# Kernel optimization log

Hardware: AMD Instinct MI355X
Metric: run time of the kernel (lower is better)

The kernel has to match this reference:

```python
import jax, jax.numpy as jnp
import numpy as np

KERNEL_MUL = 2.0
KERNEL_NUM = 5
EPS = 1e-06


def setup_inputs() -> dict:
    key = jax.random.key(0)
    k1, k2 = jax.random.split(key)
    N, D = 4096, 256
    source = jax.random.normal(k1, (N, D), dtype=jnp.float32)
    target = jax.random.normal(k2, (N, D), dtype=jnp.float32)
    return {"source": source, "target": target}


def reference(source, target):
    n_src = source.shape[0]
    total = jnp.concatenate([source, target], axis=0)  # [2N, D]
    n = total.shape[0]
    # the broadcasted (total0 - total1)**2 sum, without the O(N^2*D) tensor).
    sq = jnp.sum(total * total, axis=1)  # [2N]
    L2 = sq[:, None] + sq[None, :] - 2.0 * (total @ total.T)  # [2N, 2N]
    # Bandwidth from detached distances (torch uses L2_distance.data).
    bandwidth = jax.lax.stop_gradient(jnp.sum(L2)) / (n * n - n)
    bandwidth = bandwidth / (KERNEL_MUL ** (KERNEL_NUM // 2))
    kernels = jnp.zeros_like(L2)
    for i in range(KERNEL_NUM):
        bw = bandwidth * (KERNEL_MUL ** i)
        kernels = kernels + jnp.exp(-L2 / (bw + EPS))
    XX = kernels[:n_src, :n_src]
    YY = kernels[n_src:, n_src:]
    XY = kernels[:n_src, n_src:]
    YX = kernels[n_src:, :n_src]
    return jnp.mean(XX + YY - XY - YX)
```

## Files before the change

kernel.cpp:

```cpp
#include <hip/hip_runtime.h>

#define N_TOT 8192
#define NS 4096
#define D 256
#define NB 64
#define NTRI (NB*(NB+1)/2)
#define HALF_B 32

typedef float f32x16 __attribute__((ext_vector_type(16)));
typedef float f32x2 __attribute__((ext_vector_type(2)));
typedef short bf16x8 __attribute__((ext_vector_type(8)));

__device__ __forceinline__ void gload16(const void* g, void* l) {
  __builtin_amdgcn_global_load_lds(
      (const __attribute__((address_space(1))) unsigned int*)g,
      (__attribute__((address_space(3))) unsigned int*)l,
      16, 0, 0);
}

__device__ __forceinline__ unsigned short f2bf(float f) {
  unsigned int u = __builtin_bit_cast(unsigned int, f);
  u += 0x7FFFu + ((u >> 16) & 1u);
  return (unsigned short)(u >> 16);
}

__global__ void k_zero(float* __restrict__ colsum, float* __restrict__ S) {
  colsum[threadIdx.x] = 0.f;
  if (threadIdx.x == 0) S[0] = 0.f;
}

__global__ void k_prep(const float* __restrict__ src, const float* __restrict__ tgt,
                       unsigned short* __restrict__ Xb, float* __restrict__ sqv,
                       float* __restrict__ colsum, float* __restrict__ S) {
  __shared__ float colacc[256];
  __shared__ float wred[4];
  int t = threadIdx.x, l = t & 63, w = t >> 6;
  colacc[t] = 0.f;
  __syncthreads();
  int base = blockIdx.x * 32;
  float c0 = 0.f, c1 = 0.f, c2 = 0.f, c3 = 0.f;
  float wsq = 0.f;
  #pragma unroll
  for (int r = 0; r < 8; ++r) {
    int row = base + w * 8 + r;
    const float* p = (row < NS) ? (src + (size_t)row * D) : (tgt + (size_t)(row - NS) * D);
    float4 v = ((const float4*)p)[l];
    ushort4 bv;
    bv.x = f2bf(v.x); bv.y = f2bf(v.y); bv.z = f2bf(v.z); bv.w = f2bf(v.w);
    ((ushort4*)(Xb + (size_t)row * D))[l] = bv;
    c0 += v.x; c1 += v.y; c2 += v.z; c3 += v.w;
    float s = fmaf(v.x, v.x, fmaf(v.y, v.y, fmaf(v.z, v.z, v.w * v.w)));
    for (int o = 32; o > 0; o >>= 1) s += __shfl_down(s, o, 64);
    if (l == 0) { sqv[row] = s; wsq += s; }
  }
  atomicAdd(&colacc[4 * l + 0], c0);
  atomicAdd(&colacc[4 * l + 1], c1);
  atomicAdd(&colacc[4 * l + 2], c2);
  atomicAdd(&colacc[4 * l + 3], c3);
  if (l == 0) wred[w] = wsq;
  __syncthreads();
  atomicAdd(&colsum[t], colacc[t]);
  if (t == 0) atomicAdd(S, (wred[0] + wred[1]) + (wred[2] + wred[3]));
}

__global__ void k_bw(const float* __restrict__ colsum, const float* __restrict__ S,
                     float* __restrict__ coef) {
  __shared__ double red[256];
  int t = threadIdx.x;
  double c = (double)colsum[t];
  red[t] = c * c;
  __syncthreads();
  for (int s = 128; s > 0; s >>= 1) {
    if (t < s) red[t] += red[t + s];
    __syncthreads();
  }
  if (t == 0) {
    double msq = red[0];
    double Sv = (double)S[0];
    double n = (double)N_TOT;
    double sumL2 = 2.0 * n * Sv - 2.0 * msq;
    double bw = sumL2 / (n * n - n) / 4.0;
    double c4 = 1.0 / (bw * 16.0 + 1e-6);
    coef[0] = (float)(c4 * 1.4426950408889634);
  }
}

__global__ __launch_bounds__(256) void k_main(
    const unsigned short* __restrict__ Xb, const float* __restrict__ sqv,
    const float* __restrict__ coef, float* __restrict__ bpart) {
  int b = blockIdx.x;
  int bi = (int)((2.f * NB + 1.f - sqrtf((float)((2 * NB + 1) * (2 * NB + 1) - 8 * b))) * 0.5f);
  if (bi < 0) bi = 0;
  if (bi > NB - 1) bi = NB - 1;
  while ((bi + 1) * (2 * NB - bi) / 2 <= b) ++bi;
  while (bi * (2 * NB - bi + 1) / 2 > b) --bi;
  int bj = bi + (b - bi * (2 * NB - bi + 1) / 2);

  __shared__ unsigned short ldsA[128 * 64];
  __shared__ unsigned short ldsB[128 * 64];
  __shared__ float sqA[128], sqB[128];
  __shared__ float redw[4];

  int t = threadIdx.x, l = t & 63, w = t >> 6;
  int lr = l & 31, half = l >> 5;
  int waveRow = w >> 1, waveCol = w & 1;

  if (t < 128) sqA[t] = sqv[bi * 128 + t];
  else         sqB[t - 128] = sqv[bj * 128 + (t - 128)];
  float A4 = coef[0];

  const unsigned short* arow = Xb + (size_t)bi * 128 * D;
  const unsigned short* brow = Xb + (size_t)bj * 128 * D;

  f32x16 acc[2][2] = {};

  for (int ko = 0; ko < 4; ++ko) {
    if (ko) __syncthreads();
    int kOff = ko * 64;
    #pragma unroll
    for (int p = 0; p < 4; ++p) {
      int seg = p * 256 + w * 64 + l;
      int row = seg >> 3;
      int kb = (seg & 7) ^ (row & 7);
      int goff = row * D + kOff + kb * 8;
      gload16(arow + goff, &ldsA[(p * 4 + w) * 512]);
      gload16(brow + goff, &ldsB[(p * 4 + w) * 512]);
    }
    __syncthreads();
    #pragma unroll
    for (int ks = 0; ks < 4; ++ks) {
      int phys = (2 * ks + half) ^ (lr & 7);
      bf16x8 aF[2], bF[2];
      #pragma unroll
      for (int rb = 0; rb < 2; ++rb) {
        int rowA = waveRow * 64 + rb * 32 + lr;
        aF[rb] = *(const bf16x8*)&ldsA[rowA * 64 + phys * 8];
        int rowB = waveCol * 64 + rb * 32 + lr;
        bF[rb] = *(const bf16x8*)&ldsB[rowB * 64 + phys * 8];
      }
      #pragma unroll
      for (int rb = 0; rb < 2; ++rb)
        #pragma unroll
        for (int cb = 0; cb < 2; ++cb)
          acc[rb][cb] = __builtin_amdgcn_mfma_f32_32x32x16_bf16(aF[rb], bF[cb], acc[rb][cb], 0, 0, 0);
    }
  }

  float c2A4 = 2.f * A4, nA4 = -A4;
  f32x2 lsum2 = {0.f, 0.f};
  bool diag = (bi == bj);
  #pragma unroll
  for (int cb = 0; cb < 2; ++cb) {
    int jj = waveCol * 64 + cb * 32 + lr;
    float bjv = nA4 * sqB[jj];
    #pragma unroll
    for (int rb = 0; rb < 2; ++rb) {
      #pragma unroll
      for (int r = 0; r < 16; r += 2) {
        int ii = waveRow * 64 + rb * 32 + (r & 3) + 8 * (r >> 2) + 4 * half;
        f32x2 dot2 = {acc[rb][cb][r], acc[rb][cb][r + 1]};
        f32x2 sq2 = {sqA[ii], sqA[ii + 1]};
        f32x2 tt = c2A4 * dot2 + (nA4 * sq2 + bjv);
        f32x2 e;
        e.x = __builtin_amdgcn_exp2f(tt.x);
        e.y = __builtin_amdgcn_exp2f(tt.y);
        f32x2 e2 = e * e, e4 = e2 * e2, e8 = e4 * e4, e16 = e8 * e8;
        f32x2 kern = ((e + e2) + (e4 + e8)) + e16;
        if (diag) {
          if (ii == jj) kern.x = 0.f;
          if (ii + 1 == jj) kern.y = 0.f;
        }
        lsum2 += kern;
      }
    }
  }
  float lsum = lsum2.x + lsum2.y;
  for (int o = 32; o > 0; o >>= 1) lsum += __shfl_down(lsum, o, 64);
  if (l == 0) redw[w] = lsum;
  __syncthreads();
  if (t == 0) {
    float tot = (redw[0] + redw[1]) + (redw[2] + redw[3]);
    float wgt = diag ? 1.f : 2.f;
    float sgn = ((bi < HALF_B) == (bj < HALF_B)) ? 1.f : -1.f;
    bpart[b] = tot * wgt * sgn;
  }
}

__global__ void k_final(const float* __restrict__ bpart, float* __restrict__ out) {
  __shared__ double red[256];
  int t = threadIdx.x;
  double s = 0.0;
  for (int k = 0; k < 9; ++k) {
    int idx = k * 256 + t;
    if (idx < NTRI) s += (double)bpart[idx];
  }
  red[t] = s;
  __syncthreads();
  for (int st = 128; st > 0; st >>= 1) {
    if (t < st) red[t] += red[t + st];
    __syncthreads();
  }
  if (t == 0) {
    double total = red[0] + 5.0 * (double)N_TOT;
    out[0] = (float)(total / ((double)NS * (double)NS));
  }
}

extern "C" void kernel_launch(void* const* d_in, const int* in_sizes, int n_in,
                              void* d_out, int out_size, void* d_ws, size_t ws_size,
                              hipStream_t stream) {
  const float* src = (const float*)d_in[0];
  const float* tgt = (const float*)d_in[1];
  float* out = (float*)d_out;
  char* ws = (char*)d_ws;
  unsigned short* Xb = (unsigned short*)ws;
  float* sqv   = (float*)(ws + (4u << 20));
  float* colsum = (float*)(ws + (4u << 20) + (32u << 10));
  float* S     = (float*)(ws + (4u << 20) + (33u << 10));
  float* coef  = (float*)(ws + (4u << 20) + (34u << 10));
  float* bpart = (float*)(ws + (4u << 20) + (35u << 10));

  hipLaunchKernelGGL(k_zero, dim3(1), dim3(256), 0, stream, colsum, S);
  hipLaunchKernelGGL(k_prep, dim3(256), dim3(256), 0, stream, src, tgt, Xb, sqv, colsum, S);
  hipLaunchKernelGGL(k_bw, dim3(1), dim3(256), 0, stream, colsum, S, coef);
  hipLaunchKernelGGL(k_main, dim3(NTRI), dim3(256), 0, stream, Xb, sqv, coef, bpart);
  hipLaunchKernelGGL(k_final, dim3(1), dim3(256), 0, stream, bpart, out);
}
```

Baseline: 105.5 us.

## Double-buffer LDS tiles in main kernel and replace zero kernel with memset

The K loop of the main MFMA kernel now uses two LDS buffer pairs, so the global-to-LDS load of the next 64-wide K slice is issued before the current slice is computed. This hides load latency behind MFMA work and leaves one barrier per slice instead of two. LDS use doubles to about 64 KB per block, which can lower occupancy. The zeroing kernel is also replaced by a single hipMemsetAsync over the colsum and S buffers, which requires moving S, coef and bpart so S sits directly after colsum.

```diff
diff --git a/kernel.cpp b/kernel.cpp
--- a/kernel.cpp
+++ b/kernel.cpp
@@ -24,9 +24,42 @@
   return (unsigned short)(u >> 16);
 }
 
-__global__ void k_zero(float* __restrict__ colsum, float* __restrict__ S) {
-  colsum[threadIdx.x] = 0.f;
-  if (threadIdx.x == 0) S[0] = 0.f;
+__device__ __forceinline__ void stage_tile(const unsigned short* __restrict__ arow,
+                                           const unsigned short* __restrict__ brow,
+                                           unsigned short* bufA, unsigned short* bufB,
+                                           int kOff, int w, int l) {
+  #pragma unroll
+  for (int p = 0; p < 4; ++p) {
+    int seg = p * 256 + w * 64 + l;
+    int row = seg >> 3;
+    int kb = (seg & 7) ^ (row & 7);
+    int goff = row * D + kOff + kb * 8;
+    gload16(arow + goff, bufA + (p * 4 + w) * 512);
+    gload16(brow + goff, bufB + (p * 4 + w) * 512);
+  }
+}
+
+__device__ __forceinline__ void compute_tile(const unsigned short* LA,
+                                             const unsigned short* LB,
+                                             f32x16 acc[2][2],
+                                             int waveRow, int waveCol, int lr, int half) {
+  #pragma unroll
+  for (int ks = 0; ks < 4; ++ks) {
+    int phys = (2 * ks + half) ^ (lr & 7);
+    bf16x8 aF[2], bF[2];
+    #pragma unroll
+    for (int rb = 0; rb < 2; ++rb) {
+      int rowA = waveRow * 64 + rb * 32 + lr;
+      aF[rb] = *(const bf16x8*)&LA[rowA * 64 + phys * 8];
+      int rowB = waveCol * 64 + rb * 32 + lr;
+      bF[rb] = *(const bf16x8*)&LB[rowB * 64 + phys * 8];
+    }
+    #pragma unroll
+    for (int rb = 0; rb < 2; ++rb)
+      #pragma unroll
+      for (int cb = 0; cb < 2; ++cb)
+        acc[rb][cb] = __builtin_amdgcn_mfma_f32_32x32x16_bf16(aF[rb], bF[cb], acc[rb][cb], 0, 0, 0);
+  }
 }
 
 __global__ void k_prep(const float* __restrict__ src, const float* __restrict__ tgt,
@@ -96,8 +129,8 @@
   while (bi * (2 * NB - bi + 1) / 2 > b) --bi;
   int bj = bi + (b - bi * (2 * NB - bi + 1) / 2);
 
-  __shared__ unsigned short ldsA[128 * 64];
-  __shared__ unsigned short ldsB[128 * 64];
+  __shared__ unsigned short ldsA0[8192], ldsB0[8192];
+  __shared__ unsigned short ldsA1[8192], ldsB1[8192];
   __shared__ float sqA[128], sqB[128];
   __shared__ float redw[4];
 
@@ -105,46 +138,27 @@
   int lr = l & 31, half = l >> 5;
   int waveRow = w >> 1, waveCol = w & 1;
 
+  float A4 = coef[0];
   if (t < 128) sqA[t] = sqv[bi * 128 + t];
   else         sqB[t - 128] = sqv[bj * 128 + (t - 128)];
-  float A4 = coef[0];
 
   const unsigned short* arow = Xb + (size_t)bi * 128 * D;
   const unsigned short* brow = Xb + (size_t)bj * 128 * D;
 
   f32x16 acc[2][2] = {};
 
-  for (int ko = 0; ko < 4; ++ko) {
-    if (ko) __syncthreads();
-    int kOff = ko * 64;
-    #pragma unroll
-    for (int p = 0; p < 4; ++p) {
-      int seg = p * 256 + w * 64 + l;
-      int row = seg >> 3;
-      int kb = (seg & 7) ^ (row & 7);
-      int goff = row * D + kOff + kb * 8;
-      gload16(arow + goff, &ldsA[(p * 4 + w) * 512]);
-      gload16(brow + goff, &ldsB[(p * 4 + w) * 512]);
-    }
-    __syncthreads();
-    #pragma unroll
-    for (int ks = 0; ks < 4; ++ks) {
-      int phys = (2 * ks + half) ^ (lr & 7);
-      bf16x8 aF[2], bF[2];
-      #pragma unroll
-      for (int rb = 0; rb < 2; ++rb) {
-        int rowA = waveRow * 64 + rb * 32 + lr;
-        aF[rb] = *(const bf16x8*)&ldsA[rowA * 64 + phys * 8];
-        int rowB = waveCol * 64 + rb * 32 + lr;
-        bF[rb] = *(const bf16x8*)&ldsB[rowB * 64 + phys * 8];
-      }
-      #pragma unroll
-      for (int rb = 0; rb < 2; ++rb)
-        #pragma unroll
-        for (int cb = 0; cb < 2; ++cb)
-          acc[rb][cb] = __builtin_amdgcn_mfma_f32_32x32x16_bf16(aF[rb], bF[cb], acc[rb][cb], 0, 0, 0);
-    }
-  }
+  stage_tile(arow, brow, ldsA0, ldsB0, 0, w, l);
+  __syncthreads();
+  stage_tile(arow, brow, ldsA1, ldsB1, 64, w, l);
+  compute_tile(ldsA0, ldsB0, acc, waveRow, waveCol, lr, half);
+  __syncthreads();
+  stage_tile(arow, brow, ldsA0, ldsB0, 128, w, l);
+  compute_tile(ldsA1, ldsB1, acc, waveRow, waveCol, lr, half);
+  __syncthreads();
+  stage_tile(arow, brow, ldsA1, ldsB1, 192, w, l);
+  compute_tile(ldsA0, ldsB0, acc, waveRow, waveCol, lr, half);
+  __syncthreads();
+  compute_tile(ldsA1, ldsB1, acc, waveRow, waveCol, lr, half);
 
   float c2A4 = 2.f * A4, nA4 = -A4;
   f32x2 lsum2 = {0.f, 0.f};
@@ -216,11 +230,11 @@
   unsigned short* Xb = (unsigned short*)ws;
   float* sqv   = (float*)(ws + (4u << 20));
   float* colsum = (float*)(ws + (4u << 20) + (32u << 10));
-  float* S     = (float*)(ws + (4u << 20) + (33u << 10));
-  float* coef  = (float*)(ws + (4u << 20) + (34u << 10));
-  float* bpart = (float*)(ws + (4u << 20) + (35u << 10));
-
-  hipLaunchKernelGGL(k_zero, dim3(1), dim3(256), 0, stream, colsum, S);
+  float* S     = (float*)(ws + (4u << 20) + (32u << 10) + 1024);
+  float* coef  = (float*)(ws + (4u << 20) + (33u << 10) + 64);
+  float* bpart = (float*)(ws + (4u << 20) + (34u << 10));
+
+  hipMemsetAsync(colsum, 0, 1028, stream);
   hipLaunchKernelGGL(k_prep, dim3(256), dim3(256), 0, stream, src, tgt, Xb, sqv, colsum, S);
   hipLaunchKernelGGL(k_bw, dim3(1), dim3(256), 0, stream, colsum, S, coef);
   hipLaunchKernelGGL(k_main, dim3(NTRI), dim3(256), 0, stream, Xb, sqv, coef, bpart);
```

New measurement: 111.8 us. +6.0%, slower.
